# Kernel tuning notes

Measured on AMD Instinct MI355X. Metric: run time of the kernel, lower is better.

## Reference

```python
import jax, jax.numpy as jnp
import numpy as np
from jax import lax

NF = 64
KS = 3
PAD = 1
TOPK = 2
DG = 8          # deformable_groups
N = KS * KS     # 9 sampling points


def conv3x3(x, w, b):
    y = lax.conv_general_dilated(x, w, (1, 1), 'SAME',
                                 dimension_numbers=('NCHW', 'OIHW', 'NCHW'))
    return y + b[None, :, None, None]


def lrelu(x):
    return jnp.where(x >= 0, x, 0.1 * x)


def dsp_sample(x, feat, w_om, b_om):
    """Modulated deformable sampling (DSP_sep2): returns the N bilinearly
    sampled, mask-modulated taps per pixel, shape (B, C, N, H, W)."""
    B, C, H, W = x.shape
    Cg = C // DG
    om = conv3x3(feat, w_om, b_om)              # (B, 3*DG*N, H, W)
    o1, o2, m = jnp.split(om, 3, axis=1)
    off_y = o1.reshape(B, DG, N, H, W)
    off_x = o2.reshape(B, DG, N, H, W)
    mask = jax.nn.sigmoid(m).reshape(B, DG, 1, N, H * W)
    kk = (jnp.arange(KS) - PAD).astype(jnp.float32)
    kdy = jnp.repeat(kk, KS)                    # (N,) kernel row offsets
    kdx = jnp.tile(kk, KS)                      # (N,) kernel col offsets
    ii = jnp.arange(H, dtype=jnp.float32)
    jj = jnp.arange(W, dtype=jnp.float32)
    ys = ii[None, None, None, :, None] + kdy[None, None, :, None, None] + off_y
    xs = jj[None, None, None, None, :] + kdx[None, None, :, None, None] + off_x
    y0 = jnp.floor(ys)
    x0 = jnp.floor(xs)
    xf = x.reshape(B, DG, Cg, H * W)
    out = jnp.zeros((B, DG, Cg, N, H * W), x.dtype)
    # bilinear interpolation with zero padding outside the image
    for dy in (0.0, 1.0):
        for dx in (0.0, 1.0):
            yi = y0 + dy
            xi = x0 + dx
            wgt = (1.0 - jnp.abs(ys - yi)) * (1.0 - jnp.abs(xs - xi))
            valid = (yi >= 0) & (yi <= H - 1) & (xi >= 0) & (xi <= W - 1)
            lin = (jnp.clip(yi, 0, H - 1) * W + jnp.clip(xi, 0, W - 1)).astype(jnp.int32)
            g = jnp.take_along_axis(xf[:, :, :, None, :],
                                    lin.reshape(B, DG, 1, N, H * W), axis=-1)
            out = out + g * jnp.where(valid, wgt, 0.0).reshape(B, DG, 1, N, H * W)
    return (out * mask).reshape(B, C, N, H, W)


def setup_inputs() -> dict:
    key = jax.random.key(0)
    ks = jax.random.split(key, 9)
    B, C, H, W = 2, NF, 192, 192

    def rn(k, s, sc=1.0):
        return jax.random.normal(k, s, jnp.float32) * sc

    return {
        'query': rn(ks[0], (B, C, H, W)),
        'key':   rn(ks[1], (B, C, H, W)),
        'value': rn(ks[2], (B, C, H, W)),
        'w1': rn(ks[3], (C, 2 * C, 3, 3), 0.05), 'b1': rn(ks[4], (C,), 0.05),
        'w2': rn(ks[5], (C, C, 3, 3), 0.05),     'b2': rn(ks[6], (C,), 0.05),
        'w_om': rn(ks[7], (3 * DG * N, C, 3, 3), 0.01),
        'b_om': rn(ks[8], (3 * DG * N,), 0.01),
    }


def reference(query, key, value, w1, b1, w2, b2, w_om, b_om):
    B, C, H, W = query.shape
    HW = H * W
    feat = lrelu(conv3x3(jnp.concatenate([query, key], axis=1), w1, b1))
    feat = lrelu(conv3x3(feat, w2, b2))
    # deformable sampled keys: (B, C, N, H, W) -> (B, HW, N, C)
    key_off = dsp_sample(key, feat, w_om, b_om).transpose(0, 3, 4, 2, 1).reshape(B, HW, N, C)
    q = query.reshape(B, C, HW).transpose(0, 2, 1)            # (B, HW, C)
    rel = jnp.einsum('bpnc,bpc->bpn', key_off, q)             # relevance scores
    topv, topi = lax.top_k(rel, TOPK)                         # (B, HW, TOPK)
    corr = jax.nn.softmax(topv, axis=-1)
    val_off = dsp_sample(value, feat, w_om, b_om).transpose(0, 3, 4, 2, 1).reshape(B, HW, N, C)
    k_sel = jnp.take_along_axis(key_off, topi[..., None], axis=2)  # (B, HW, TOPK, C)
    v_sel = jnp.take_along_axis(val_off, topi[..., None], axis=2)
    k_upd = jnp.einsum('bptc,bpt->bpc', k_sel, corr)
    v_out = jnp.einsum('bptc,bpt->bpc', v_sel, corr).transpose(0, 2, 1)  # (B, C, HW)
    weight = jnp.einsum('bpc,bpc->bp', q, k_upd)              # (B, HW)
    return (weight, v_out)
```

## Files before the change

### kernel.cpp

```cpp
#include <hip/hip_runtime.h>
#include <math.h>

#define H_  192
#define W_  192
#define HW_ (192 * 192)
#define B_  2
#define C_  64

typedef __attribute__((ext_vector_type(8))) short short8;
typedef __attribute__((ext_vector_type(4))) short short4v;
typedef __attribute__((ext_vector_type(4))) float float4v;

__device__ __forceinline__ unsigned short f2bf(float f) {
    unsigned u = __float_as_uint(f);
    u += 0x7FFFu + ((u >> 16) & 1u);
    return (unsigned short)(u >> 16);
}
__device__ __forceinline__ float bf2f(unsigned short h) {
    return __uint_as_float((unsigned)h << 16);
}
__device__ __forceinline__ void split3(float x, short& h, short& m, short& l) {
    unsigned short hh = f2bf(x);
    float r1 = x - bf2f(hh);
    unsigned short mm = f2bf(r1);
    float r2 = r1 - bf2f(mm);
    unsigned short ll = f2bf(r2);
    h = (short)hh; m = (short)mm; l = (short)ll;
}

__device__ __forceinline__ float bilin_dot(const float* __restrict__ pl,
                                           float ys, float xs, int c4,
                                           float4v q4) {
    float y0 = floorf(ys), x0 = floorf(xs);
    float fy = ys - y0, fx = xs - x0;
    int iy = (int)y0, ix = (int)x0;
    float acc = 0.f;
    #pragma unroll
    for (int dy = 0; dy < 2; ++dy) {
        #pragma unroll
        for (int dx = 0; dx < 2; ++dx) {
            int yy = iy + dy, xx = ix + dx;
            float wgt = (dy ? fy : 1.f - fy) * (dx ? fx : 1.f - fx);
            bool valid = (yy >= 0) && (yy < H_) && (xx >= 0) && (xx < W_);
            int yc = min(max(yy, 0), H_ - 1);
            int xc = min(max(xx, 0), W_ - 1);
            const float4v v = *(const float4v*)(pl + (size_t)(yc * W_ + xc) * 64 + c4);
            float d = v[0] * q4[0] + v[1] * q4[1] + v[2] * q4[2] + v[3] * q4[3];
            acc += valid ? wgt * d : 0.f;
        }
    }
    return acc;
}
__device__ __forceinline__ float4v bilin_v4(const float* __restrict__ pl,
                                            float ys, float xs, int c4) {
    float y0 = floorf(ys), x0 = floorf(xs);
    float fy = ys - y0, fx = xs - x0;
    int iy = (int)y0, ix = (int)x0;
    float4v acc;
    acc[0] = acc[1] = acc[2] = acc[3] = 0.f;
    #pragma unroll
    for (int dy = 0; dy < 2; ++dy) {
        #pragma unroll
        for (int dx = 0; dx < 2; ++dx) {
            int yy = iy + dy, xx = ix + dx;
            float wgt = (dy ? fy : 1.f - fy) * (dx ? fx : 1.f - fx);
            bool valid = (yy >= 0) && (yy < H_) && (xx >= 0) && (xx < W_);
            float wz = valid ? wgt : 0.f;
            int yc = min(max(yy, 0), H_ - 1);
            int xc = min(max(xx, 0), W_ - 1);
            const float4v v = *(const float4v*)(pl + (size_t)(yc * W_ + xc) * 64 + c4);
            #pragma unroll
            for (int r = 0; r < 4; ++r) acc[r] += wz * v[r];
        }
    }
    return acc;
}

__global__ __launch_bounds__(256) void prep_w_k(
    const float* __restrict__ w1, const float* __restrict__ w2,
    const float* __restrict__ wom,
    short* __restrict__ pw1, short* __restrict__ pw2, short* __restrict__ pwom)
{
    int idx = blockIdx.x * 256 + threadIdx.x;
    int arr;
    if (idx < 144 * 512) { arr = 0; }
    else if (idx < (144 + 72) * 512) { arr = 1; idx -= 144 * 512; }
    else if (idx < (144 + 72 + 252) * 512) { arr = 2; idx -= (144 + 72) * 512; }
    else return;
    int frag = idx >> 9, within = idx & 511;
    int lane = within >> 3, j = within & 7;
    int KS   = (arr == 0) ? 4 : 2;
    int mt   = frag / (9 * KS);
    int rem  = frag % (9 * KS);
    int kk   = rem / KS;
    int s    = rem % KS;
    int co   = mt * 16 + (lane & 15);
    int c    = s * 32 + (lane >> 4) * 8 + j;
    float v = 0.f;
    if (arr == 0)      v = w1[(co * 128 + c) * 9 + kk];
    else if (arr == 1) v = w2[(co * 64 + c) * 9 + kk];
    else if (co < 216) v = wom[(co * 64 + c) * 9 + kk];
    short h, m, l;
    split3(v, h, m, l);
    short* dst = (arr == 0) ? pw1 : (arr == 1) ? pw2 : pwom;
    size_t base = (size_t)frag * 1536 + lane * 8 + j;
    dst[base]        = h;
    dst[base + 512]  = m;
    dst[base + 1024] = l;
}

__global__ __launch_bounds__(256) void nchw_to_nhwc(
    const float* __restrict__ key, const float* __restrict__ value,
    float* __restrict__ kT, float* __restrict__ vT)
{
    __shared__ float sm[64][65];
    const int tid = threadIdx.x;
    const int p0  = blockIdx.x * 64;
    const int b   = blockIdx.y;
    const float* src = blockIdx.z ? value : key;
    float*       dst = blockIdx.z ? vT    : kT;
    const int pp = tid & 63;
    const int r0 = tid >> 6;
    #pragma unroll
    for (int c = r0; c < 64; c += 4)
        sm[c][pp] = src[(size_t)(b * 64 + c) * HW_ + p0 + pp];
    __syncthreads();
    const int cc = tid & 63;
    #pragma unroll
    for (int pw = r0; pw < 64; pw += 4)
        dst[((size_t)b * HW_ + p0 + pw) * 64 + cc] = sm[cc][pw];
}

template<int CIN, int MT, bool LRELU, int OUTMODE, bool FROMF32>
__global__ __launch_bounds__(256) void conv_mfma(
    const void* __restrict__ in0v, const void* __restrict__ in1v,
    const short* __restrict__ pw, const float* __restrict__ bias,
    void* __restrict__ outv)
{
    constexpr int KS   = CIN / 32;
    constexpr int MTW  = MT / 2;
    constexpr int LSTR = 104;
    __shared__ __align__(16) short smem[66 * LSTR];

    const int tid  = threadIdx.x;
    const int lane = tid & 63;
    const int w    = tid >> 6;
    const int wh   = w & 1;
    const int wn   = w >> 1;
    const int quad = lane >> 4;
    const int nn   = lane & 15;

    const int flat = blockIdx.x;
    const int xcd  = flat & 7;
    const int cc_  = flat >> 3;
    const int b    = xcd >> 2;
    const int r4   = xcd & 3;
    const int i    = r4 * 48 + cc_ / 3;
    const int j0   = (cc_ % 3) * 64;
    const int mt0  = wh * MTW;

    float4v acc[MTW][2];
    #pragma unroll
    for (int m = 0; m < MTW; ++m)
        #pragma unroll
        for (int t = 0; t < 2; ++t)
            #pragma unroll
            for (int r = 0; r < 4; ++r) acc[m][t][r] = 0.f;

    for (int ky = 0; ky < 3; ++ky) {
        const int row = i + ky - 1;
        const bool rowok = (row >= 0) && (row < H_);
        for (int s = 0; s < KS; ++s) {
            __syncthreads();
            if (FROMF32) {
                const float* src = (s < KS / 2) ? (const float*)in0v
                                                : (const float*)in1v;
                const int cbase = (s & (KS / 2 - 1)) * 32;
                for (int idx = tid; idx < 32 * 66; idx += 256) {
                    int ci = idx / 66, px = idx - ci * 66;
                    int col = j0 - 1 + px;
                    float v = 0.f;
                    if (rowok && col >= 0 && col < W_)
                        v = src[(size_t)(b * 64 + cbase + ci) * HW_ + row * W_ + col];
                    short h, m, l;
                    split3(v, h, m, l);
                    smem[px * LSTR + ci]      = h;
                    smem[px * LSTR + 32 + ci] = m;
                    smem[px * LSTR + 64 + ci] = l;
                }
            } else {
                const short* src = (const short*)in0v
                                 + (size_t)b * HW_ * (3 * CIN);
                for (int idx = tid; idx < 66 * 24; idx += 256) {
                    int px = idx / 24, r = idx - px * 24;
                    int limb = r >> 3, dq = r & 7;
                    int col = j0 - 1 + px;
                    unsigned long long v = 0;
                    if (rowok && col >= 0 && col < W_)
                        v = *(const unsigned long long*)(src
                              + (size_t)(row * W_ + col) * (3 * CIN)
                              + limb * CIN + s * 32 + dq * 4);
                    *(unsigned long long*)(&smem[px * LSTR + limb * 32 + dq * 4]) = v;
                }
            }
            __syncthreads();

            #pragma unroll
            for (int kx = 0; kx < 3; ++kx) {
                const int kk = ky * 3 + kx;
                short8 bh[2], bm[2], bl[2];
                #pragma unroll
                for (int t2 = 0; t2 < 2; ++t2) {
                    const int t = wn * 2 + t2;
                    const short* bp = &smem[(t * 16 + nn + kx) * LSTR + quad * 8];
                    bh[t2] = *(const short8*)bp;
                    bm[t2] = *(const short8*)(bp + 32);
                    bl[t2] = *(const short8*)(bp + 64);
                }
                #pragma unroll
                for (int m = 0; m < MTW; ++m) {
                    const short* ap = pw
                        + ((size_t)(((mt0 + m) * 9 + kk) * KS + s)) * 1536
                        + lane * 8;
                    short8 ah = *(const short8*)ap;
                    short8 am = *(const short8*)(ap + 512);
                    short8 al = *(const short8*)(ap + 1024);
                    #pragma unroll
                    for (int t2 = 0; t2 < 2; ++t2) {
                        acc[m][t2] = __builtin_amdgcn_mfma_f32_16x16x32_bf16(ah, bh[t2], acc[m][t2], 0, 0, 0);
                        acc[m][t2] = __builtin_amdgcn_mfma_f32_16x16x32_bf16(ah, bm[t2], acc[m][t2], 0, 0, 0);
                        acc[m][t2] = __builtin_amdgcn_mfma_f32_16x16x32_bf16(am, bh[t2], acc[m][t2], 0, 0, 0);
                        acc[m][t2] = __builtin_amdgcn_mfma_f32_16x16x32_bf16(am, bm[t2], acc[m][t2], 0, 0, 0);
                        acc[m][t2] = __builtin_amdgcn_mfma_f32_16x16x32_bf16(ah, bl[t2], acc[m][t2], 0, 0, 0);
                        acc[m][t2] = __builtin_amdgcn_mfma_f32_16x16x32_bf16(al, bh[t2], acc[m][t2], 0, 0, 0);
                    }
                }
            }
        }
    }

    #pragma unroll
    for (int m = 0; m < MTW; ++m) {
        const int co0 = (mt0 + m) * 16 + quad * 4;
        #pragma unroll
        for (int t2 = 0; t2 < 2; ++t2) {
            const int t = wn * 2 + t2;
            const int p = i * W_ + j0 + t * 16 + nn;
            if (OUTMODE == 0) {
                short* feat = (short*)outv;
                short4v hv, mv, lv;
                #pragma unroll
                for (int r = 0; r < 4; ++r) {
                    float x = acc[m][t2][r] + bias[co0 + r];
                    if (LRELU) x = (x >= 0.f) ? x : 0.1f * x;
                    short h, mm, l;
                    split3(x, h, mm, l);
                    hv[r] = h; mv[r] = mm; lv[r] = l;
                }
                short* dp = feat + ((size_t)b * HW_ + p) * 192 + co0;
                *(short4v*)dp         = hv;
                *(short4v*)(dp + 64)  = mv;
                *(short4v*)(dp + 128) = lv;
            } else {
                if (co0 < 216) {
                    float* om = (float*)outv;
                    float4v v;
                    #pragma unroll
                    for (int r = 0; r < 4; ++r)
                        v[r] = acc[m][t2][r] + bias[co0 + r];
                    *(float4v*)(om + ((size_t)b * HW_ + p) * 216 + co0) = v;
                }
            }
        }
    }
}

__global__ __launch_bounds__(256) void sampler_k(
    const float* __restrict__ query, const float* __restrict__ kT,
    const float* __restrict__ vT, const float* __restrict__ om,
    float* __restrict__ out_w, float* __restrict__ out_v)
{
    __shared__ float sq[16 * 68];
    const int tid  = threadIdx.x;
    const int bb   = blockIdx.x;
    const int b    = bb / 2304;
    const int pblk = (bb - b * 2304) * 16;

    #pragma unroll
    for (int k = 0; k < 4; ++k) {
        int idx = tid + k * 256;
        int c   = idx >> 4;
        int px  = idx & 15;
        sq[px * 68 + c] = query[(size_t)(b * 64 + c) * HW_ + pblk + px];
    }
    __syncthreads();

    const int lane   = tid & 63;
    const int w      = tid >> 6;
    const int px_sub = lane >> 4;
    const int cl     = lane & 15;
    const int c4     = cl * 4;
    const int g      = cl >> 1;
    const int p      = pblk + w * 4 + px_sub;
    const int i      = p / W_;
    const int j      = p - i * W_;

    const float4v q4 = *(const float4v*)&sq[(w * 4 + px_sub) * 68 + c4];

    const float* omb = om + ((size_t)b * HW_ + p) * 216;
    float offy[9], offx[9], mk[9];
    #pragma unroll
    for (int n = 0; n < 9; ++n) {
        offy[n] = omb[g * 9 + n];
        offx[n] = omb[72 + g * 9 + n];
        float mv = omb[144 + g * 9 + n];
        mk[n] = 1.f / (1.f + expf(-mv));
    }

    const float* kpl = kT + (size_t)b * HW_ * 64;
    float rel[9];
    #pragma unroll
    for (int n = 0; n < 9; ++n) {
        float ys = (float)i + (float)(n / 3 - 1) + offy[n];
        float xs = (float)j + (float)(n % 3 - 1) + offx[n];
        float d = bilin_dot(kpl, ys, xs, c4, q4) * mk[n];
        #pragma unroll
        for (int off = 1; off < 16; off <<= 1)
            d += __shfl_xor(d, off, 64);
        rel[n] = d;
    }

    int n0 = 0; float v0 = rel[0];
    #pragma unroll
    for (int n = 1; n < 9; ++n) { if (rel[n] > v0) { v0 = rel[n]; n0 = n; } }
    int n1 = -1; float v1 = -1e30f;
    #pragma unroll
    for (int n = 0; n < 9; ++n) { if (n != n0 && rel[n] > v1) { v1 = rel[n]; n1 = n; } }

    float e1  = expf(v1 - v0);
    float inv = 1.f / (1.f + e1);
    float c0 = inv, c1 = e1 * inv;

    if (cl == 0) out_w[(size_t)b * HW_ + p] = c0 * v0 + c1 * v1;

    float oy0 = 0, ox0 = 0, m0 = 0, oy1 = 0, ox1 = 0, m1 = 0;
    #pragma unroll
    for (int n = 0; n < 9; ++n) {
        if (n == n0) { oy0 = offy[n]; ox0 = offx[n]; m0 = mk[n]; }
        if (n == n1) { oy1 = offy[n]; ox1 = offx[n]; m1 = mk[n]; }
    }

    const float* vpl = vT + (size_t)b * HW_ * 64;
    float ys0 = (float)i + (float)(n0 / 3 - 1) + oy0;
    float xs0 = (float)j + (float)(n0 % 3 - 1) + ox0;
    float ys1 = (float)i + (float)(n1 / 3 - 1) + oy1;
    float xs1 = (float)j + (float)(n1 % 3 - 1) + ox1;
    float4v vv0 = bilin_v4(vpl, ys0, xs0, c4);
    float4v vv1 = bilin_v4(vpl, ys1, xs1, c4);
    float w0 = c0 * m0, w1s = c1 * m1;
    #pragma unroll
    for (int r = 0; r < 4; ++r)
        out_v[(size_t)(b * C_ + c4 + r) * HW_ + p] = w0 * vv0[r] + w1s * vv1[r];
}

extern "C" void kernel_launch(void* const* d_in, const int* in_sizes, int n_in,
                              void* d_out, int out_size, void* d_ws, size_t ws_size,
                              hipStream_t stream)
{
    const float* query = (const float*)d_in[0];
    const float* key   = (const float*)d_in[1];
    const float* value = (const float*)d_in[2];
    const float* w1    = (const float*)d_in[3];
    const float* b1    = (const float*)d_in[4];
    const float* w2    = (const float*)d_in[5];
    const float* b2    = (const float*)d_in[6];
    const float* wom   = (const float*)d_in[7];
    const float* bom   = (const float*)d_in[8];
    float* out = (float*)d_out;

    char* ws = (char*)d_ws;
    short* f1  = (short*)(ws);
    float* om  = (float*)(ws);
    short* f2  = (short*)(ws + 63700992);
    float* kT  = (float*)(ws + 63700992);
    float* vT  = (float*)(ws + 82575360);
    short* pwom= (short*)(ws + 92012544);
    short* pw1 = (short*)(ws + 92786688);
    short* pw2 = (short*)(ws + 93229056);

    prep_w_k<<<936, 256, 0, stream>>>(w1, w2, wom, pw1, pw2, pwom);

    conv_mfma<128, 4,  true,  0, true ><<<1152, 256, 0, stream>>>(query, key, pw1, b1, (void*)f1);
    conv_mfma<64,  4,  true,  0, false><<<1152, 256, 0, stream>>>(f1, nullptr, pw2, b2, (void*)f2);
    conv_mfma<64,  14, false, 1, false><<<1152, 256, 0, stream>>>(f2, nullptr, pwom, bom, (void*)om);

    nchw_to_nhwc<<<dim3(576, B_, 2), 256, 0, stream>>>(key, value, kT, vT);

    float* out_w = out;
    float* out_v = out + (size_t)B_ * HW_;
    sampler_k<<<(B_ * HW_) / 16, 256, 0, stream>>>(query, kT, vT, om, out_w, out_v);
}
```

Baseline: 433.8 us.

## Double-buffer conv input staging and interleave MFMA accumulator chains

```diff
diff --git a/kernel.cpp b/kernel.cpp
--- a/kernel.cpp
+++ b/kernel.cpp
@@ -140,7 +140,8 @@
     constexpr int KS   = CIN / 32;
     constexpr int MTW  = MT / 2;
     constexpr int LSTR = 104;
-    __shared__ __align__(16) short smem[66 * LSTR];
+    constexpr int NPH  = 3 * KS;
+    __shared__ __align__(16) short smem[2][66 * LSTR];
 
     const int tid  = threadIdx.x;
     const int lane = tid & 63;
@@ -167,76 +168,127 @@
             #pragma unroll
             for (int r = 0; r < 4; ++r) acc[m][t][r] = 0.f;
 
-    for (int ky = 0; ky < 3; ++ky) {
+    float fbuf[9];
+    unsigned long long pbuf[7];
+
+    auto stage_load = [&](int ph) {
+        const int ky  = ph / KS, s = ph % KS;
         const int row = i + ky - 1;
-        const bool rowok = (row >= 0) && (row < H_);
-        for (int s = 0; s < KS; ++s) {
-            __syncthreads();
-            if (FROMF32) {
-                const float* src = (s < KS / 2) ? (const float*)in0v
-                                                : (const float*)in1v;
-                const int cbase = (s & (KS / 2 - 1)) * 32;
-                for (int idx = tid; idx < 32 * 66; idx += 256) {
+        const bool rok = (row >= 0) && (row < H_);
+        if constexpr (FROMF32) {
+            const float* src = (s < KS / 2) ? (const float*)in0v
+                                            : (const float*)in1v;
+            const int cbase = (s & (KS / 2 - 1)) * 32;
+            #pragma unroll
+            for (int k = 0; k < 9; ++k) {
+                int idx = tid + k * 256;
+                float v = 0.f;
+                if (idx < 32 * 66) {
                     int ci = idx / 66, px = idx - ci * 66;
                     int col = j0 - 1 + px;
-                    float v = 0.f;
-                    if (rowok && col >= 0 && col < W_)
+                    if (rok && col >= 0 && col < W_)
                         v = src[(size_t)(b * 64 + cbase + ci) * HW_ + row * W_ + col];
-                    short h, m, l;
-                    split3(v, h, m, l);
-                    smem[px * LSTR + ci]      = h;
-                    smem[px * LSTR + 32 + ci] = m;
-                    smem[px * LSTR + 64 + ci] = l;
-                }
-            } else {
-                const short* src = (const short*)in0v
-                                 + (size_t)b * HW_ * (3 * CIN);
-                for (int idx = tid; idx < 66 * 24; idx += 256) {
+                }
+                fbuf[k] = v;
+            }
+        } else {
+            const short* src = (const short*)in0v + (size_t)b * HW_ * (3 * CIN);
+            #pragma unroll
+            for (int k = 0; k < 7; ++k) {
+                int idx = tid + k * 256;
+                unsigned long long v = 0;
+                if (idx < 66 * 24) {
                     int px = idx / 24, r = idx - px * 24;
                     int limb = r >> 3, dq = r & 7;
                     int col = j0 - 1 + px;
-                    unsigned long long v = 0;
-                    if (rowok && col >= 0 && col < W_)
+                    if (rok && col >= 0 && col < W_)
                         v = *(const unsigned long long*)(src
                               + (size_t)(row * W_ + col) * (3 * CIN)
                               + limb * CIN + s * 32 + dq * 4);
-                    *(unsigned long long*)(&smem[px * LSTR + limb * 32 + dq * 4]) = v;
-                }
-            }
+                }
+                pbuf[k] = v;
+            }
+        }
+    };
+    auto stage_write = [&](int nb) {
+        if constexpr (FROMF32) {
+            #pragma unroll
+            for (int k = 0; k < 9; ++k) {
+                int idx = tid + k * 256;
+                if (idx < 32 * 66) {
+                    int ci = idx / 66, px = idx - ci * 66;
+                    short h, m, l;
+                    split3(fbuf[k], h, m, l);
+                    short* d = &smem[nb][px * LSTR + ci];
+                    d[0]  = h;
+                    d[32] = m;
+                    d[64] = l;
+                }
+            }
+        } else {
+            #pragma unroll
+            for (int k = 0; k < 7; ++k) {
+                int idx = tid + k * 256;
+                if (idx < 66 * 24) {
+                    int px = idx / 24, r = idx - px * 24;
+                    int limb = r >> 3, dq = r & 7;
+                    *(unsigned long long*)(&smem[nb][px * LSTR + limb * 32 + dq * 4]) = pbuf[k];
+                }
+            }
+        }
+    };
+
+    stage_load(0);
+    stage_write(0);
+    __syncthreads();
+
+    int cur = 0;
+    for (int ph = 0; ph < NPH; ++ph) {
+        const int ky = ph / KS;
+        const int s  = ph % KS;
+
+        if (ph + 1 < NPH) stage_load(ph + 1);
+
+        #pragma unroll
+        for (int kx = 0; kx < 3; ++kx) {
+            const int kk = ky * 3 + kx;
+            short8 bh[2], bm[2], bl[2];
+            #pragma unroll
+            for (int t2 = 0; t2 < 2; ++t2) {
+                const int t = wn * 2 + t2;
+                const short* bp = &smem[cur][(t * 16 + nn + kx) * LSTR + quad * 8];
+                bh[t2] = *(const short8*)bp;
+                bm[t2] = *(const short8*)(bp + 32);
+                bl[t2] = *(const short8*)(bp + 64);
+            }
+            #pragma unroll
+            for (int m = 0; m < MTW; ++m) {
+                const short* ap = pw
+                    + ((size_t)(((mt0 + m) * 9 + kk) * KS + s)) * 1536
+                    + lane * 8;
+                short8 ah = *(const short8*)ap;
+                short8 am = *(const short8*)(ap + 512);
+                short8 al = *(const short8*)(ap + 1024);
+                acc[m][0] = __builtin_amdgcn_mfma_f32_16x16x32_bf16(ah, bh[0], acc[m][0], 0, 0, 0);
+                acc[m][1] = __builtin_amdgcn_mfma_f32_16x16x32_bf16(ah, bh[1], acc[m][1], 0, 0, 0);
+                acc[m][0] = __builtin_amdgcn_mfma_f32_16x16x32_bf16(ah, bm[0], acc[m][0], 0, 0, 0);
+                acc[m][1] = __builtin_amdgcn_mfma_f32_16x16x32_bf16(ah, bm[1], acc[m][1], 0, 0, 0);
+                acc[m][0] = __builtin_amdgcn_mfma_f32_16x16x32_bf16(am, bh[0], acc[m][0], 0, 0, 0);
+                acc[m][1] = __builtin_amdgcn_mfma_f32_16x16x32_bf16(am, bh[1], acc[m][1], 0, 0, 0);
+                acc[m][0] = __builtin_amdgcn_mfma_f32_16x16x32_bf16(am, bm[0], acc[m][0], 0, 0, 0);
+                acc[m][1] = __builtin_amdgcn_mfma_f32_16x16x32_bf16(am, bm[1], acc[m][1], 0, 0, 0);
+                acc[m][0] = __builtin_amdgcn_mfma_f32_16x16x32_bf16(ah, bl[0], acc[m][0], 0, 0, 0);
+                acc[m][1] = __builtin_amdgcn_mfma_f32_16x16x32_bf16(ah, bl[1], acc[m][1], 0, 0, 0);
+                acc[m][0] = __builtin_amdgcn_mfma_f32_16x16x32_bf16(al, bh[0], acc[m][0], 0, 0, 0);
+                acc[m][1] = __builtin_amdgcn_mfma_f32_16x16x32_bf16(al, bh[1], acc[m][1], 0, 0, 0);
+            }
+        }
+
+        if (ph + 1 < NPH) {
+            stage_write(cur ^ 1);
             __syncthreads();
-
-            #pragma unroll
-            for (int kx = 0; kx < 3; ++kx) {
-                const int kk = ky * 3 + kx;
-                short8 bh[2], bm[2], bl[2];
-                #pragma unroll
-                for (int t2 = 0; t2 < 2; ++t2) {
-                    const int t = wn * 2 + t2;
-                    const short* bp = &smem[(t * 16 + nn + kx) * LSTR + quad * 8];
-                    bh[t2] = *(const short8*)bp;
-                    bm[t2] = *(const short8*)(bp + 32);
-                    bl[t2] = *(const short8*)(bp + 64);
-                }
-                #pragma unroll
-                for (int m = 0; m < MTW; ++m) {
-                    const short* ap = pw
-                        + ((size_t)(((mt0 + m) * 9 + kk) * KS + s)) * 1536
-                        + lane * 8;
-                    short8 ah = *(const short8*)ap;
-                    short8 am = *(const short8*)(ap + 512);
-                    short8 al = *(const short8*)(ap + 1024);
-                    #pragma unroll
-                    for (int t2 = 0; t2 < 2; ++t2) {
-                        acc[m][t2] = __builtin_amdgcn_mfma_f32_16x16x32_bf16(ah, bh[t2], acc[m][t2], 0, 0, 0);
-                        acc[m][t2] = __builtin_amdgcn_mfma_f32_16x16x32_bf16(ah, bm[t2], acc[m][t2], 0, 0, 0);
-                        acc[m][t2] = __builtin_amdgcn_mfma_f32_16x16x32_bf16(am, bh[t2], acc[m][t2], 0, 0, 0);
-                        acc[m][t2] = __builtin_amdgcn_mfma_f32_16x16x32_bf16(am, bm[t2], acc[m][t2], 0, 0, 0);
-                        acc[m][t2] = __builtin_amdgcn_mfma_f32_16x16x32_bf16(ah, bl[t2], acc[m][t2], 0, 0, 0);
-                        acc[m][t2] = __builtin_amdgcn_mfma_f32_16x16x32_bf16(al, bh[t2], acc[m][t2], 0, 0, 0);
-                    }
-                }
-            }
-        }
+        }
+        cur ^= 1;
     }
 
     #pragma unroll
```

After: 496.0 us. 1.14x slower.

## Replace 3-limb bf16 split GEMM with 2-limb scaled fp16 split

Applied to the files above, without the earlier changes.

```diff
diff --git a/kernel.cpp b/kernel.cpp
--- a/kernel.cpp
+++ b/kernel.cpp
@@ -10,22 +10,16 @@
 typedef __attribute__((ext_vector_type(8))) short short8;
 typedef __attribute__((ext_vector_type(4))) short short4v;
 typedef __attribute__((ext_vector_type(4))) float float4v;
-
-__device__ __forceinline__ unsigned short f2bf(float f) {
-    unsigned u = __float_as_uint(f);
-    u += 0x7FFFu + ((u >> 16) & 1u);
-    return (unsigned short)(u >> 16);
-}
-__device__ __forceinline__ float bf2f(unsigned short h) {
-    return __uint_as_float((unsigned)h << 16);
-}
-__device__ __forceinline__ void split3(float x, short& h, short& m, short& l) {
-    unsigned short hh = f2bf(x);
-    float r1 = x - bf2f(hh);
-    unsigned short mm = f2bf(r1);
-    float r2 = r1 - bf2f(mm);
-    unsigned short ll = f2bf(r2);
-    h = (short)hh; m = (short)mm; l = (short)ll;
+typedef _Float16 __attribute__((ext_vector_type(8))) half8;
+
+union hbits { _Float16 f; short s; };
+__device__ __forceinline__ void split2(float x, short& h, short& l) {
+    _Float16 hf = (_Float16)x;
+    float r = (x - (float)hf) * 4096.f;
+    _Float16 lf = (_Float16)r;
+    hbits u;
+    u.f = hf; h = u.s;
+    u.f = lf; l = u.s;
 }
 
 __device__ __forceinline__ float bilin_dot(const float* __restrict__ pl,
@@ -100,13 +94,12 @@
     if (arr == 0)      v = w1[(co * 128 + c) * 9 + kk];
     else if (arr == 1) v = w2[(co * 64 + c) * 9 + kk];
     else if (co < 216) v = wom[(co * 64 + c) * 9 + kk];
-    short h, m, l;
-    split3(v, h, m, l);
+    short h, l;
+    split2(v, h, l);
     short* dst = (arr == 0) ? pw1 : (arr == 1) ? pw2 : pwom;
-    size_t base = (size_t)frag * 1536 + lane * 8 + j;
-    dst[base]        = h;
-    dst[base + 512]  = m;
-    dst[base + 1024] = l;
+    size_t base = (size_t)frag * 1024 + lane * 8 + j;
+    dst[base]       = h;
+    dst[base + 512] = l;
 }
 
 __global__ __launch_bounds__(256) void nchw_to_nhwc(
@@ -139,7 +132,7 @@
 {
     constexpr int KS   = CIN / 32;
     constexpr int MTW  = MT / 2;
-    constexpr int LSTR = 104;
+    constexpr int LSTR = 72;
     __shared__ __align__(16) short smem[66 * LSTR];
 
     const int tid  = threadIdx.x;
@@ -159,13 +152,13 @@
     const int j0   = (cc_ % 3) * 64;
     const int mt0  = wh * MTW;
 
-    float4v acc[MTW][2];
+    float4v accM[MTW][2], accC[MTW][2];
     #pragma unroll
     for (int m = 0; m < MTW; ++m)
         #pragma unroll
         for (int t = 0; t < 2; ++t)
             #pragma unroll
-            for (int r = 0; r < 4; ++r) acc[m][t][r] = 0.f;
+            for (int r = 0; r < 4; ++r) { accM[m][t][r] = 0.f; accC[m][t][r] = 0.f; }
 
     for (int ky = 0; ky < 3; ++ky) {
         const int row = i + ky - 1;
@@ -182,23 +175,22 @@
                     float v = 0.f;
                     if (rowok && col >= 0 && col < W_)
                         v = src[(size_t)(b * 64 + cbase + ci) * HW_ + row * W_ + col];
-                    short h, m, l;
-                    split3(v, h, m, l);
+                    short h, l;
+                    split2(v, h, l);
                     smem[px * LSTR + ci]      = h;
-                    smem[px * LSTR + 32 + ci] = m;
-                    smem[px * LSTR + 64 + ci] = l;
+                    smem[px * LSTR + 32 + ci] = l;
                 }
             } else {
                 const short* src = (const short*)in0v
-                                 + (size_t)b * HW_ * (3 * CIN);
-                for (int idx = tid; idx < 66 * 24; idx += 256) {
-                    int px = idx / 24, r = idx - px * 24;
+                                 + (size_t)b * HW_ * (2 * CIN);
+                for (int idx = tid; idx < 66 * 16; idx += 256) {
+                    int px = idx >> 4, r = idx & 15;
                     int limb = r >> 3, dq = r & 7;
                     int col = j0 - 1 + px;
                     unsigned long long v = 0;
                     if (rowok && col >= 0 && col < W_)
                         v = *(const unsigned long long*)(src
-                              + (size_t)(row * W_ + col) * (3 * CIN)
+                              + (size_t)(row * W_ + col) * (2 * CIN)
                               + limb * CIN + s * 32 + dq * 4);
                     *(unsigned long long*)(&smem[px * LSTR + limb * 32 + dq * 4]) = v;
                 }
@@ -208,37 +200,33 @@
             #pragma unroll
             for (int kx = 0; kx < 3; ++kx) {
                 const int kk = ky * 3 + kx;
-                short8 bh[2], bm[2], bl[2];
+                half8 bh[2], bl[2];
                 #pragma unroll
                 for (int t2 = 0; t2 < 2; ++t2) {
                     const int t = wn * 2 + t2;
                     const short* bp = &smem[(t * 16 + nn + kx) * LSTR + quad * 8];
-                    bh[t2] = *(const short8*)bp;
-                    bm[t2] = *(const short8*)(bp + 32);
-                    bl[t2] = *(const short8*)(bp + 64);
+                    bh[t2] = *(const half8*)bp;
+                    bl[t2] = *(const half8*)(bp + 32);
                 }
                 #pragma unroll
                 for (int m = 0; m < MTW; ++m) {
                     const short* ap = pw
-                        + ((size_t)(((mt0 + m) * 9 + kk) * KS + s)) * 1536
+                        + ((size_t)(((mt0 + m) * 9 + kk) * KS + s)) * 1024
                         + lane * 8;
-                    short8 ah = *(const short8*)ap;
-                    short8 am = *(const short8*)(ap + 512);
-                    short8 al = *(const short8*)(ap + 1024);
-                    #pragma unroll
-                    for (int t2 = 0; t2 < 2; ++t2) {
-                        acc[m][t2] = __builtin_amdgcn_mfma_f32_16x16x32_bf16(ah, bh[t2], acc[m][t2], 0, 0, 0);
-                        acc[m][t2] = __builtin_amdgcn_mfma_f32_16x16x32_bf16(ah, bm[t2], acc[m][t2], 0, 0, 0);
-                        acc[m][t2] = __builtin_amdgcn_mfma_f32_16x16x32_bf16(am, bh[t2], acc[m][t2], 0, 0, 0);
-                        acc[m][t2] = __builtin_amdgcn_mfma_f32_16x16x32_bf16(am, bm[t2], acc[m][t2], 0, 0, 0);
-                        acc[m][t2] = __builtin_amdgcn_mfma_f32_16x16x32_bf16(ah, bl[t2], acc[m][t2], 0, 0, 0);
-                        acc[m][t2] = __builtin_amdgcn_mfma_f32_16x16x32_bf16(al, bh[t2], acc[m][t2], 0, 0, 0);
-                    }
+                    half8 ah = *(const half8*)ap;
+                    half8 al = *(const half8*)(ap + 512);
+                    accM[m][0] = __builtin_amdgcn_mfma_f32_16x16x32_f16(ah, bh[0], accM[m][0], 0, 0, 0);
+                    accM[m][1] = __builtin_amdgcn_mfma_f32_16x16x32_f16(ah, bh[1], accM[m][1], 0, 0, 0);
+                    accC[m][0] = __builtin_amdgcn_mfma_f32_16x16x32_f16(ah, bl[0], accC[m][0], 0, 0, 0);
+                    accC[m][1] = __builtin_amdgcn_mfma_f32_16x16x32_f16(ah, bl[1], accC[m][1], 0, 0, 0);
+                    accC[m][0] = __builtin_amdgcn_mfma_f32_16x16x32_f16(al, bh[0], accC[m][0], 0, 0, 0);
+                    accC[m][1] = __builtin_amdgcn_mfma_f32_16x16x32_f16(al, bh[1], accC[m][1], 0, 0, 0);
                 }
             }
         }
     }
 
+    constexpr float CSC = 1.f / 4096.f;
     #pragma unroll
     for (int m = 0; m < MTW; ++m) {
         const int co0 = (mt0 + m) * 16 + quad * 4;
@@ -248,26 +236,25 @@
             const int p = i * W_ + j0 + t * 16 + nn;
             if (OUTMODE == 0) {
                 short* feat = (short*)outv;
-                short4v hv, mv, lv;
+                short4v hv, lv;
                 #pragma unroll
                 for (int r = 0; r < 4; ++r) {
-                    float x = acc[m][t2][r] + bias[co0 + r];
+                    float x = accM[m][t2][r] + accC[m][t2][r] * CSC + bias[co0 + r];
                     if (LRELU) x = (x >= 0.f) ? x : 0.1f * x;
-                    short h, mm, l;
-                    split3(x, h, mm, l);
-                    hv[r] = h; mv[r] = mm; lv[r] = l;
-                }
-                short* dp = feat + ((size_t)b * HW_ + p) * 192 + co0;
-                *(short4v*)dp         = hv;
-                *(short4v*)(dp + 64)  = mv;
-                *(short4v*)(dp + 128) = lv;
+                    short h, l;
+                    split2(x, h, l);
+                    hv[r] = h; lv[r] = l;
+                }
+                short* dp = feat + ((size_t)b * HW_ + p) * 128 + co0;
+                *(short4v*)dp        = hv;
+                *(short4v*)(dp + 64) = lv;
             } else {
                 if (co0 < 216) {
                     float* om = (float*)outv;
                     float4v v;
                     #pragma unroll
                     for (int r = 0; r < 4; ++r)
-                        v[r] = acc[m][t2][r] + bias[co0 + r];
+                        v[r] = accM[m][t2][r] + accC[m][t2][r] * CSC + bias[co0 + r];
                     *(float4v*)(om + ((size_t)b * HW_ + p) * 216 + co0) = v;
                 }
             }
```

New measurement: 450.2 us. +3.8%, slower.
